# Optimization experiments

Hardware: AMD Instinct MI355X
Metric: run time of the kernel (lower is better)

## Reference

```python
import jax, jax.numpy as jnp
import numpy as np

B, S, H = 8, 8192, 1024
CAPACITY_FACTOR = 0.5


def setup_inputs() -> dict:
    key = jax.random.key(0)
    ks = jax.random.split(key, 5)
    sc = lambda fan: np.float32(1.0 / np.sqrt(fan))
    return {
        "x": jax.random.normal(ks[0], (B, S, H), dtype=jnp.float32),
        # router: Linear(H, H//4) -> ReLU -> Linear(H//4, 1)
        "W1": jax.random.normal(ks[1], (H, H // 4), dtype=jnp.float32) * sc(H),
        "b1": jnp.zeros((H // 4,), dtype=jnp.float32),
        "W2": jax.random.normal(ks[2], (H // 4, 1), dtype=jnp.float32) * sc(H // 4),
        "b2": jnp.zeros((1,), dtype=jnp.float32),
        # external layer_fn realized as a dense layer: gelu(x @ Wl)
        "Wl": jax.random.normal(ks[3], (H, H), dtype=jnp.float32) * sc(H),
    }


def reference(x, W1, b1, W2, b2, Wl):
    # router scores [B, S, 1]
    scores = jax.nn.relu(jnp.einsum("bsh,hd->bsd", x, W1) + b1)
    scores = jnp.einsum("bsd,do->bso", scores, W2) + b2
    routing_weights = jax.nn.sigmoid(scores)  # [B, S, 1]

    # eval path: process only top-capacity tokens per batch row
    capacity = int(S * CAPACITY_FACTOR)
    _, top_idx = jax.lax.top_k(scores[..., 0], capacity)  # [B, C]

    selected = jnp.take_along_axis(x, top_idx[..., None], axis=1)  # [B, C, H]
    processed = jax.nn.gelu(jnp.einsum("bch,hd->bcd", selected, Wl))  # layer_fn

    batch_idx = jnp.arange(x.shape[0])[:, None]  # [B, 1]
    output = x.at[batch_idx, top_idx].set(processed)  # scatter back into clone of x
    return output, routing_weights
```

## Files before the change

kernel.cpp:

```cpp
#include <hip/hip_runtime.h>
#include <stdint.h>

#define B_   8
#define S_   8192
#define H_   1024
#define HQ_  256
#define CAP_ 4096
#define UCAP_ (S_-CAP_)
#define M_   (B_*CAP_)
#define EPSB 0.012f
#define LCAP 8192

using f32x4 = __attribute__((ext_vector_type(4))) float;
using s16x8 = __attribute__((ext_vector_type(8))) short;

__device__ __forceinline__ unsigned short f2bf(float f) {
  unsigned u = __float_as_uint(f);
  u += 0x7FFF + ((u >> 16) & 1);
  return (unsigned short)(u >> 16);
}
__device__ __forceinline__ float bf2f(unsigned short h) {
  return __uint_as_float(((unsigned)h) << 16);
}

__device__ __forceinline__ float gelu_f(float v) {
  float s = v + 0.044715f * v * v * v;
  float e = __expf(-1.5957691216057308f * s);
  return v * __builtin_amdgcn_rcpf(1.0f + e);
}

__device__ __forceinline__ unsigned mono(float f) {
  unsigned u = __float_as_uint(f);
  return (u & 0x80000000u) ? ~u : (u | 0x80000000u);
}
__device__ __forceinline__ float unmono(unsigned k) {
  unsigned u = (k & 0x80000000u) ? (k & 0x7fffffffu) : ~k;
  return __uint_as_float(u);
}

__device__ __forceinline__ void gload_lds16(const void* g, void* l) {
  __builtin_amdgcn_global_load_lds(
      (const __attribute__((address_space(1))) void*)(uintptr_t)g,
      (__attribute__((address_space(3))) void*)(uintptr_t)l,
      16, 0, 0);
}

__device__ __forceinline__ float radix_select_T(
    const float* __restrict__ srow, unsigned* hist,
    unsigned* sh_b, unsigned* sh_gt, int tid) {
  unsigned prefix = 0; int plen = 0; unsigned rank = CAP_;
  #pragma unroll
  for (int round = 0; round < 3; ++round) {
    const int nb = (round < 2) ? 11 : 10;
    hist[tid] = 0; hist[tid + 1024] = 0;
    __syncthreads();
    for (int i = tid; i < S_; i += 1024) {
      unsigned k = mono(srow[i]);
      if (plen == 0 || (k >> (32 - plen)) == prefix) {
        unsigned bucket = (k << plen) >> (32 - nb);
        atomicAdd(&hist[bucket], 1u);
      }
    }
    __syncthreads();
    for (int s = 1; s < 2048; s <<= 1) {
      unsigned t0 = (tid + s < 2048) ? hist[tid + s] : 0;
      unsigned t1 = (tid + 1024 + s < 2048) ? hist[tid + 1024 + s] : 0;
      __syncthreads();
      hist[tid] += t0; hist[tid + 1024] += t1;
      __syncthreads();
    }
    #pragma unroll
    for (int h = 0; h < 2; ++h) {
      int i = tid + h * 1024;
      unsigned ge = hist[i];
      unsigned gt = (i < 2047) ? hist[i + 1] : 0;
      if (gt < rank && rank <= ge) { *sh_b = (unsigned)i; *sh_gt = gt; }
    }
    __syncthreads();
    prefix = (prefix << nb) | *sh_b;
    plen += nb;
    rank -= *sh_gt;
    __syncthreads();
  }
  return unmono(prefix);
}

__global__ __launch_bounds__(256) void prep_w1_kernel(
    const float* __restrict__ W1, unsigned short* __restrict__ w1t_hi) {
  __shared__ float tile[32][33];
  const int n0 = blockIdx.x * 32, k0 = blockIdx.y * 32;
  const int tx = threadIdx.x, ty = threadIdx.y;
  for (int i = ty; i < 32; i += 8) tile[i][tx] = W1[(size_t)(k0 + i) * HQ_ + n0 + tx];
  __syncthreads();
  for (int i = ty; i < 32; i += 8)
    w1t_hi[(size_t)(n0 + i) * H_ + k0 + tx] = f2bf(tile[tx][i]);
}

__global__ __launch_bounds__(512) void router_mfma_kernel(
    const float* __restrict__ x, const unsigned short* __restrict__ w1t_hi,
    const float* __restrict__ b1, const float* __restrict__ W2,
    const float* __restrict__ b2, float* __restrict__ scores,
    float* __restrict__ rw) {
  __shared__ __align__(16) unsigned short AsH[128 * 64];
  __shared__ __align__(16) unsigned short BsH[256 * 64];
  __shared__ float part[128][4];
  const int t = threadIdx.x;
  const int lane = t & 63, w = t >> 6;
  const int m0 = blockIdx.x * 128;
  const int wr = w >> 2, wc = w & 3;
  const int r16 = lane & 15, ks = lane >> 4;

  const float* aptr[4];
  int aso[4];
  #pragma unroll
  for (int u = 0; u < 4; ++u) {
    int idx = t + u * 512;
    int row = idx >> 4, q = idx & 15;
    aptr[u] = x + (size_t)(m0 + row) * H_ + q * 4;
    aso[u] = row * 64 + (((q >> 1) ^ (row & 7)) << 3) + (q & 1) * 4;
  }
  const unsigned short* bptr[4];
  int bdst[4];
  #pragma unroll
  for (int u = 0; u < 4; ++u) {
    int c0 = u * 512 + w * 64;
    int c = c0 + lane;
    int row = c >> 3, sl = c & 7;
    int slz = sl ^ (row & 7);
    bptr[u] = w1t_hi + (size_t)row * H_ + slz * 8;
    bdst[u] = c0 * 8;
  }

  f32x4 acc[4][4];
  #pragma unroll
  for (int i = 0; i < 4; ++i)
    #pragma unroll
    for (int j = 0; j < 4; ++j) acc[i][j] = (f32x4){0.f, 0.f, 0.f, 0.f};

  for (int k0 = 0; k0 < H_; k0 += 64) {
    float4 av[4];
    #pragma unroll
    for (int u = 0; u < 4; ++u) av[u] = *(const float4*)(aptr[u] + k0);
    #pragma unroll
    for (int u = 0; u < 4; ++u) gload_lds16(bptr[u] + k0, &BsH[bdst[u]]);
    #pragma unroll
    for (int u = 0; u < 4; ++u) {
      ushort4 hh;
      hh.x = f2bf(av[u].x); hh.y = f2bf(av[u].y);
      hh.z = f2bf(av[u].z); hh.w = f2bf(av[u].w);
      *(ushort4*)&AsH[aso[u]] = hh;
    }
    __syncthreads();
    #pragma unroll
    for (int kk = 0; kk < 2; ++kk) {
      const int g = kk * 4 + ks;
      s16x8 ah[4], bh[4];
      #pragma unroll
      for (int i = 0; i < 4; ++i) {
        int r = wr * 64 + i * 16 + r16;
        ah[i] = *(const s16x8*)&AsH[r * 64 + (g ^ (r & 7)) * 8];
      }
      #pragma unroll
      for (int j = 0; j < 4; ++j) {
        int r = wc * 64 + j * 16 + r16;
        bh[j] = *(const s16x8*)&BsH[r * 64 + (g ^ (r & 7)) * 8];
      }
      #pragma unroll
      for (int i = 0; i < 4; ++i)
        #pragma unroll
        for (int j = 0; j < 4; ++j)
          acc[i][j] = __builtin_amdgcn_mfma_f32_16x16x32_bf16(ah[i], bh[j], acc[i][j], 0, 0, 0);
    }
    __syncthreads();
  }

  float b1v[4], w2v[4];
  #pragma unroll
  for (int j = 0; j < 4; ++j) {
    int n = wc * 64 + j * 16 + r16;
    b1v[j] = b1[n]; w2v[j] = W2[n];
  }
  const int g4 = lane >> 4;
  #pragma unroll
  for (int i = 0; i < 4; ++i) {
    #pragma unroll
    for (int r = 0; r < 4; ++r) {
      float p = 0.f;
      #pragma unroll
      for (int j = 0; j < 4; ++j) {
        float h = acc[i][j][r] + b1v[j];
        h = fmaxf(h, 0.f);
        p = fmaf(h, w2v[j], p);
      }
      p += __shfl_xor(p, 1);
      p += __shfl_xor(p, 2);
      p += __shfl_xor(p, 4);
      p += __shfl_xor(p, 8);
      if (r16 == 0) part[wr * 64 + i * 16 + g4 * 4 + r][wc] = p;
    }
  }
  __syncthreads();
  if (t < 128) {
    float sc = part[t][0] + part[t][1] + part[t][2] + part[t][3] + b2[0];
    scores[m0 + t] = sc;
    rw[m0 + t] = 1.f / (1.f + expf(-sc));
  }
}

__global__ __launch_bounds__(1024) void select_band_kernel(
    const float* __restrict__ scores, int* __restrict__ list,
    int* __restrict__ count) {
  __shared__ unsigned hist[2048];
  __shared__ unsigned sh_b, sh_gt;
  const int b = blockIdx.x;
  const int tid = threadIdx.x;
  const float* srow = scores + (size_t)b * S_;
  const float T = radix_select_T(srow, hist, &sh_b, &sh_gt, tid);
  for (int i = tid; i < S_; i += 1024) {
    float s = srow[i];
    if (fabsf(s - T) <= EPSB) {
      int p = atomicAdd(count, 1);
      if (p < LCAP) list[p] = b * S_ + i;
    }
  }
}

__global__ __launch_bounds__(256) void recompute_kernel(
    const float* __restrict__ x, const float* __restrict__ W1,
    const float* __restrict__ b1, const float* __restrict__ W2,
    const float* __restrict__ b2, const int* __restrict__ list,
    const int* __restrict__ count, float* __restrict__ scores,
    float* __restrict__ rw) {
  __shared__ float xr[4][H_];
  __shared__ float red[4][4];
  int n = *count; if (n > LCAP) n = LCAP;
  const int j = threadIdx.x;
  for (int base = blockIdx.x * 4; base < n; base += gridDim.x * 4) {
    int nt = n - base; if (nt > 4) nt = 4;
    for (int tt = 0; tt < 4; ++tt) {
      int tok = list[base + ((tt < nt) ? tt : 0)];
      const float* xrow = x + (size_t)tok * H_;
      for (int k = j; k < H_; k += 256) xr[tt][k] = xrow[k];
    }
    __syncthreads();
    float a0 = 0.f, a1 = 0.f, a2 = 0.f, a3 = 0.f;
    for (int k = 0; k < H_; ++k) {
      float wv = W1[(size_t)k * HQ_ + j];
      a0 = fmaf(xr[0][k], wv, a0);
      a1 = fmaf(xr[1][k], wv, a1);
      a2 = fmaf(xr[2][k], wv, a2);
      a3 = fmaf(xr[3][k], wv, a3);
    }
    float aa[4] = {a0, a1, a2, a3};
    #pragma unroll
    for (int tt = 0; tt < 4; ++tt) {
      float h = fmaxf(aa[tt] + b1[j], 0.f);
      float v = h * W2[j];
      v += __shfl_xor(v, 1);  v += __shfl_xor(v, 2);  v += __shfl_xor(v, 4);
      v += __shfl_xor(v, 8);  v += __shfl_xor(v, 16); v += __shfl_xor(v, 32);
      if ((j & 63) == 0) red[tt][j >> 6] = v;
    }
    __syncthreads();
    if (j < nt) {
      int tok = list[base + j];
      float sc = red[j][0] + red[j][1] + red[j][2] + red[j][3] + b2[0];
      scores[tok] = sc;
      rw[tok] = 1.f / (1.f + expf(-sc));
    }
    __syncthreads();
  }
}

__global__ __launch_bounds__(1024) void compact_kernel(
    const float* __restrict__ scores, int* __restrict__ comp,
    int* __restrict__ ucomp) {
  __shared__ unsigned hist[2048];
  __shared__ unsigned sh_b, sh_gt;
  __shared__ int wc_eq[16], wc_sel[16], red[16];
  const int b = blockIdx.x;
  const float* srow = scores + (size_t)b * S_;
  const int tid = threadIdx.x, lane = tid & 63, wid = tid >> 6;
  const float T = radix_select_T(srow, hist, &sh_b, &sh_gt, tid);

  int cgt = 0;
  #pragma unroll
  for (int c = 0; c < 8; ++c) cgt += (srow[c * 1024 + tid] > T) ? 1 : 0;
  cgt += __shfl_xor(cgt, 1);  cgt += __shfl_xor(cgt, 2);  cgt += __shfl_xor(cgt, 4);
  cgt += __shfl_xor(cgt, 8);  cgt += __shfl_xor(cgt, 16); cgt += __shfl_xor(cgt, 32);
  if (lane == 0) red[wid] = cgt;
  __syncthreads();
  int cnt_gt = 0;
  #pragma unroll
  for (int i = 0; i < 16; ++i) cnt_gt += red[i];
  const int need = CAP_ - cnt_gt;

  int* crow = comp + b * CAP_;
  int* urow = ucomp + b * UCAP_;
  int sel_base = 0, unsel_base = 0, eq_base = 0;
  __syncthreads();
  for (int c = 0; c < 8; ++c) {
    int idx = c * 1024 + tid;
    float s = srow[idx];
    bool gt = s > T, eq = (s == T);
    unsigned long long meq = __ballot(eq);
    if (lane == 0) wc_eq[wid] = __popcll(meq);
    __syncthreads();
    int eq_off = eq_base, eq_tot = 0;
    #pragma unroll
    for (int w2 = 0; w2 < 16; ++w2) { if (w2 < wid) eq_off += wc_eq[w2]; eq_tot += wc_eq[w2]; }
    int eqpos = eq_off + __popcll(meq & ((1ull << lane) - 1));
    bool take = gt || (eq && eqpos < need);
    unsigned long long mt = __ballot(take);
    if (lane == 0) wc_sel[wid] = __popcll(mt);
    __syncthreads();
    int sel_off = sel_base, sel_tot = 0;
    #pragma unroll
    for (int w2 = 0; w2 < 16; ++w2) { if (w2 < wid) sel_off += wc_sel[w2]; sel_tot += wc_sel[w2]; }
    if (take) {
      crow[sel_off + __popcll(mt & ((1ull << lane) - 1))] = idx;
    } else {
      int un_off = unsel_base + wid * 64 - (sel_off - sel_base);
      urow[un_off + __popcll(~mt & ((1ull << lane) - 1))] = idx;
    }
    sel_base += sel_tot; unsel_base += 1024 - sel_tot; eq_base += eq_tot;
    __syncthreads();
  }
}

__global__ __launch_bounds__(256) void copy_unsel_kernel(
    const float* __restrict__ x, const int* __restrict__ ucomp,
    float* __restrict__ out) {
  int i = blockIdx.x;
  int b = i >> 12, r = i & (UCAP_ - 1);
  int token = ucomp[b * UCAP_ + r];
  size_t row = (size_t)b * S_ + token;
  const float4* src = (const float4*)(x + row * H_);
  float4* dst = (float4*)(out + row * H_);
  dst[threadIdx.x] = src[threadIdx.x];
}

__global__ __launch_bounds__(256) void wlt_kernel(
    const float* __restrict__ wl, unsigned short* __restrict__ wlt) {
  __shared__ float tile[32][33];
  const int x0 = blockIdx.x * 32, y0 = blockIdx.y * 32;
  const int tx = threadIdx.x, ty = threadIdx.y;
  for (int i = ty; i < 32; i += 8) tile[i][tx] = wl[(size_t)(y0 + i) * H_ + x0 + tx];
  __syncthreads();
  for (int i = ty; i < 32; i += 8)
    wlt[(size_t)(x0 + i) * H_ + y0 + tx] = f2bf(tile[tx][i]);
}

__global__ __launch_bounds__(256) void gather_cast_kernel(
    const float* __restrict__ x, const int* __restrict__ comp,
    unsigned short* __restrict__ xg) {
  int tid = blockIdx.x * 256 + threadIdx.x;
  int rowc = tid >> 8;
  int c4 = tid & 255;
  int b = rowc >> 12, cc = rowc & (CAP_ - 1);
  int token = comp[b * CAP_ + cc];
  float4 v = *(const float4*)&x[((size_t)(b * S_ + token)) * H_ + c4 * 4];
  ushort4 o;
  o.x = f2bf(v.x); o.y = f2bf(v.y); o.z = f2bf(v.z); o.w = f2bf(v.w);
  *(ushort4*)&xg[(size_t)rowc * H_ + c4 * 4] = o;
}

#define ISSUE_A(P, KT, BUF) do {                                               \
    int row_ = half * 128 + (P) * 32 + rr;                                     \
    int slz_ = sl ^ (row_ & 7);                                                \
    gload_lds16(xg + (size_t)(m0 + row_) * H_ + (KT) * 64 + slz_ * 8,          \
                &As[BUF][row_ * 64 + sl * 8]);                                 \
  } while (0)
#define ISSUE_B(P, KT, BUF) do {                                               \
    int row_ = half * 128 + (P) * 32 + rr;                                     \
    int slz_ = sl ^ (row_ & 7);                                                \
    gload_lds16(wlt + (size_t)(n0 + row_) * H_ + (KT) * 64 + slz_ * 8,         \
                &Bs[BUF][row_ * 64 + sl * 8]);                                 \
  } while (0)
#define MOE_PHASE(P, ISSUE, WAITSTR) do {                                      \
    s16x8 af[2][2];                                                            \
    _Pragma("unroll")                                                          \
    for (int i = 0; i < 2; ++i)                                                \
      _Pragma("unroll")                                                        \
      for (int kk = 0; kk < 2; ++kk) {                                         \
        int r_ = wr * 128 + (2 * (P) + i) * 16 + r16;                          \
        af[i][kk] = *(const s16x8*)&As[c_][r_ * 64 + ((kk * 4 + ks) ^ (r_ & 7)) * 8]; \
      }                                                                        \
    if ((P) == 0) {                                                            \
      _Pragma("unroll")                                                        \
      for (int j = 0; j < 4; ++j)                                              \
        _Pragma("unroll")                                                      \
        for (int kk = 0; kk < 2; ++kk) {                                       \
          int r_ = wc * 64 + j * 16 + r16;                                     \
          bfr[j][kk] = *(const s16x8*)&Bs[c_][r_ * 64 + ((kk * 4 + ks) ^ (r_ & 7)) * 8]; \
        }                                                                      \
    }                                                                          \
    ISSUE                                                                      \
    __builtin_amdgcn_s_barrier();                                              \
    asm volatile("s_waitcnt lgkmcnt(0)" ::: "memory");                         \
    __builtin_amdgcn_sched_barrier(0);                                         \
    __builtin_amdgcn_s_setprio(1);                                             \
    _Pragma("unroll")                                                          \
    for (int i = 0; i < 2; ++i)                                                \
      _Pragma("unroll")                                                        \
      for (int j = 0; j < 4; ++j)                                              \
        _Pragma("unroll")                                                      \
        for (int kk = 0; kk < 2; ++kk)                                         \
          acc[2 * (P) + i][j] = __builtin_amdgcn_mfma_f32_16x16x32_bf16(       \
              af[i][kk], bfr[j][kk], acc[2 * (P) + i][j], 0, 0, 0);            \
    __builtin_amdgcn_s_setprio(0);                                             \
    __builtin_amdgcn_sched_barrier(0);                                         \
    asm volatile("s_waitcnt " WAITSTR ::: "memory");                           \
    __builtin_amdgcn_s_barrier();                                              \
    __builtin_amdgcn_sched_barrier(0);                                         \
  } while (0)

__global__ __launch_bounds__(512, 1) void moe_gemm_kernel(
    const unsigned short* __restrict__ xg, const unsigned short* __restrict__ wlt,
    const int* __restrict__ comp, float* __restrict__ out) {
  __shared__ __align__(16) unsigned short As[2][256 * 64];
  __shared__ __align__(16) unsigned short Bs[2][256 * 64];
  __shared__ int toks[256];
  const int t = threadIdx.x;
  const int lane = t & 63, w = t >> 6;
  const int bid = blockIdx.x;
  const int xcd = bid & 7, wb = bid >> 3;
  const int m0 = (xcd * 16 + (wb >> 2)) * 256;
  const int n0 = (wb & 3) * 256;
  const int bb = m0 >> 12;
  if (t < 256) toks[t] = comp[bb * CAP_ + (m0 & (CAP_ - 1)) + t];
  const int wr = w >> 2, wc = w & 3;
  const int r16 = lane & 15, ks = lane >> 4;
  const int half = t >> 8, rr = (t >> 3) & 31, sl = t & 7;

  f32x4 acc[8][4];
  #pragma unroll
  for (int i = 0; i < 8; ++i)
    #pragma unroll
    for (int j = 0; j < 4; ++j) acc[i][j] = (f32x4){0.f, 0.f, 0.f, 0.f};

  ISSUE_B(0, 0, 0); ISSUE_B(1, 0, 0); ISSUE_B(2, 0, 0); ISSUE_B(3, 0, 0);
  ISSUE_A(0, 0, 0); ISSUE_A(1, 0, 0); ISSUE_A(2, 0, 0); ISSUE_A(3, 0, 0);
  asm volatile("s_waitcnt vmcnt(3)" ::: "memory");
  __syncthreads();

  for (int kt = 0; kt < 15; ++kt) {
    const int c_ = kt & 1, nb_ = c_ ^ 1;
    const int kn = kt + 1;
    s16x8 bfr[4][2];
    MOE_PHASE(0, { ISSUE_B(0, kn, nb_); ISSUE_B(1, kn, nb_); }, "vmcnt(4)");
    MOE_PHASE(1, { ISSUE_B(2, kn, nb_); ISSUE_B(3, kn, nb_); }, "vmcnt(5)");
    MOE_PHASE(2, { ISSUE_A(0, kn, nb_); ISSUE_A(1, kn, nb_); }, "vmcnt(6)");
    MOE_PHASE(3, { ISSUE_A(2, kn, nb_); ISSUE_A(3, kn, nb_); }, "vmcnt(3)");
  }
  {
    const int c_ = 1;
    s16x8 bfr[4][2];
    MOE_PHASE(0, {;}, "vmcnt(2)");
    MOE_PHASE(1, {;}, "vmcnt(1)");
    MOE_PHASE(2, {;}, "vmcnt(0)");
    MOE_PHASE(3, {;}, "vmcnt(63)");
  }

  const int g4 = lane >> 4;
  #pragma unroll
  for (int i = 0; i < 8; ++i) {
    #pragma unroll
    for (int r = 0; r < 4; ++r) {
      int rl = wr * 128 + i * 16 + g4 * 4 + r;
      int token = toks[rl];
      float* orow = out + ((size_t)(bb * S_ + token)) * H_ + n0 + wc * 64;
      #pragma unroll
      for (int j = 0; j < 4; ++j)
        orow[j * 16 + r16] = gelu_f(acc[i][j][r]);
    }
  }
}

extern "C" void kernel_launch(void* const* d_in, const int* in_sizes, int n_in,
                              void* d_out, int out_size, void* d_ws, size_t ws_size,
                              hipStream_t stream) {
  const float* x  = (const float*)d_in[0];
  const float* W1 = (const float*)d_in[1];
  const float* b1 = (const float*)d_in[2];
  const float* W2 = (const float*)d_in[3];
  const float* b2 = (const float*)d_in[4];
  const float* Wl = (const float*)d_in[5];
  float* out = (float*)d_out;
  float* rw  = out + (size_t)B_ * S_ * H_;

  char* ws = (char*)d_ws;
  float* scores        = (float*)ws;
  int*   comp          = (int*)(ws + (256 << 10));
  int*   count         = (int*)(ws + (384 << 10) + 256);
  int*   list          = (int*)(ws + (384 << 10) + 512);
  int*   ucomp         = (int*)(ws + (448 << 10));
  unsigned short* wlt  = (unsigned short*)(ws + (1 << 20));
  unsigned short* xg   = (unsigned short*)(ws + (3 << 20));
  unsigned short* w1t_hi = xg;

  hipMemsetAsync(count, 0, sizeof(int), stream);
  hipLaunchKernelGGL(prep_w1_kernel, dim3(HQ_/32, H_/32), dim3(32, 8), 0, stream,
                     W1, w1t_hi);
  hipLaunchKernelGGL(router_mfma_kernel, dim3((B_*S_)/128), dim3(512), 0, stream,
                     x, w1t_hi, b1, W2, b2, scores, rw);
  hipLaunchKernelGGL(select_band_kernel, dim3(B_), dim3(1024), 0, stream,
                     scores, list, count);
  hipLaunchKernelGGL(recompute_kernel, dim3(128), dim3(256), 0, stream,
                     x, W1, b1, W2, b2, list, count, scores, rw);
  hipLaunchKernelGGL(compact_kernel, dim3(B_), dim3(1024), 0, stream,
                     scores, comp, ucomp);
  hipLaunchKernelGGL(copy_unsel_kernel, dim3(B_*UCAP_), dim3(256), 0, stream,
                     x, ucomp, out);
  hipLaunchKernelGGL(wlt_kernel, dim3(H_/32, H_/32), dim3(32, 8), 0, stream, Wl, wlt);
  hipLaunchKernelGGL(gather_cast_kernel, dim3(M_*H_/4/256), dim3(256), 0, stream,
                     x, comp, xg);
  hipLaunchKernelGGL(moe_gemm_kernel, dim3((M_/256)*(H_/256)), dim3(512), 0, stream,
                     xg, wlt, comp, out);
}
```

Measured before the change: 395.6 us.

## Pipeline router GEMM with double-buffered direct-to-LDS loads and merge small kernels

The router GEMM now double-buffers both A (fp32 x, loaded directly to LDS and cast to bf16 at fragment-read time) and B tiles, using explicit vmcnt waits, barriers and setprio to overlap global loads with MFMA. The W1 and Wl transpose kernels are merged into one prep kernel, the gather/cast and unselected-row copy kernels are merged into one launch, and the count memset moves into the router kernel. This aims to hide memory latency in the router and cut launch overhead, at the cost of more LDS (fp32 A tile, two buffers) and occupancy limited to one block per CU.

```diff
diff --git a/kernel.cpp b/kernel.cpp
--- a/kernel.cpp
+++ b/kernel.cpp
@@ -85,93 +85,126 @@
   return unmono(prefix);
 }
 
-__global__ __launch_bounds__(256) void prep_w1_kernel(
-    const float* __restrict__ W1, unsigned short* __restrict__ w1t_hi) {
+__global__ __launch_bounds__(256) void prep_kernel(
+    const float* __restrict__ W1, unsigned short* __restrict__ w1t_hi,
+    const float* __restrict__ wl, unsigned short* __restrict__ wlt) {
   __shared__ float tile[32][33];
-  const int n0 = blockIdx.x * 32, k0 = blockIdx.y * 32;
+  const int bid = blockIdx.x;
   const int tx = threadIdx.x, ty = threadIdx.y;
-  for (int i = ty; i < 32; i += 8) tile[i][tx] = W1[(size_t)(k0 + i) * HQ_ + n0 + tx];
-  __syncthreads();
-  for (int i = ty; i < 32; i += 8)
-    w1t_hi[(size_t)(n0 + i) * H_ + k0 + tx] = f2bf(tile[tx][i]);
-}
-
-__global__ __launch_bounds__(512) void router_mfma_kernel(
+  if (bid < 256) {
+    int n0 = (bid & 7) * 32, k0 = (bid >> 3) * 32;
+    for (int i = ty; i < 32; i += 8) tile[i][tx] = W1[(size_t)(k0 + i) * HQ_ + n0 + tx];
+    __syncthreads();
+    for (int i = ty; i < 32; i += 8)
+      w1t_hi[(size_t)(n0 + i) * H_ + k0 + tx] = f2bf(tile[tx][i]);
+  } else {
+    int idx = bid - 256;
+    int x0 = (idx & 31) * 32, y0 = (idx >> 5) * 32;
+    for (int i = ty; i < 32; i += 8) tile[i][tx] = wl[(size_t)(y0 + i) * H_ + x0 + tx];
+    __syncthreads();
+    for (int i = ty; i < 32; i += 8)
+      wlt[(size_t)(x0 + i) * H_ + y0 + tx] = f2bf(tile[tx][i]);
+  }
+}
+
+#define RIA(U, KT, BUF) do {                                                   \
+    int c_i = (U) * 512 + t;                                                   \
+    int row_ = c_i >> 4, q_ = c_i & 15;                                        \
+    int qz_ = q_ ^ (row_ & 15);                                                \
+    gload_lds16(x + (size_t)(m0 + row_) * H_ + (KT) * 64 + qz_ * 4,            \
+                &Af[BUF][(size_t)c_i * 4]);                                    \
+  } while (0)
+#define RIB(U, KT, BUF) do {                                                   \
+    int row_ = (U) * 64 + (t >> 3);                                            \
+    int sl_ = t & 7;                                                           \
+    int slz_ = sl_ ^ (row_ & 7);                                               \
+    gload_lds16(w1t_hi + (size_t)row_ * H_ + (KT) * 64 + slz_ * 8,             \
+                &Bs[BUF][(size_t)row_ * 64 + sl_ * 8]);                        \
+  } while (0)
+#define RPH(P, ISSUE, WAITCODE) do {                                           \
+    s16x8 af[2];                                                               \
+    _Pragma("unroll")                                                          \
+    for (int kk = 0; kk < 2; ++kk) {                                           \
+      int r_ = wr * 64 + (P) * 16 + r16;                                       \
+      int g2 = 2 * (kk * 4 + ks);                                              \
+      float4 f0 = *(const float4*)&Af[c_][((size_t)r_ * 16 + (g2 ^ (r_ & 15))) * 4];       \
+      float4 f1 = *(const float4*)&Af[c_][((size_t)r_ * 16 + ((g2 + 1) ^ (r_ & 15))) * 4]; \
+      unsigned short hh[8];                                                    \
+      hh[0] = f2bf(f0.x); hh[1] = f2bf(f0.y); hh[2] = f2bf(f0.z); hh[3] = f2bf(f0.w); \
+      hh[4] = f2bf(f1.x); hh[5] = f2bf(f1.y); hh[6] = f2bf(f1.z); hh[7] = f2bf(f1.w); \
+      af[kk] = *(s16x8*)hh;                                                    \
+    }                                                                          \
+    if ((P) == 0) {                                                            \
+      _Pragma("unroll")                                                        \
+      for (int j = 0; j < 4; ++j)                                              \
+        _Pragma("unroll")                                                      \
+        for (int kk = 0; kk < 2; ++kk) {                                       \
+          int r_ = wc * 64 + j * 16 + r16;                                     \
+          bfr[j][kk] = *(const s16x8*)&Bs[c_][(size_t)r_ * 64 + ((kk * 4 + ks) ^ (r_ & 7)) * 8]; \
+        }                                                                      \
+    }                                                                          \
+    ISSUE                                                                      \
+    __builtin_amdgcn_s_barrier();                                              \
+    asm volatile("s_waitcnt lgkmcnt(0)" ::: "memory");                         \
+    __builtin_amdgcn_sched_barrier(0);                                         \
+    __builtin_amdgcn_s_setprio(1);                                             \
+    _Pragma("unroll")                                                          \
+    for (int j = 0; j < 4; ++j)                                                \
+      _Pragma("unroll")                                                        \
+      for (int kk = 0; kk < 2; ++kk)                                           \
+        acc[P][j] = __builtin_amdgcn_mfma_f32_16x16x32_bf16(                   \
+            af[kk], bfr[j][kk], acc[P][j], 0, 0, 0);                           \
+    __builtin_amdgcn_s_setprio(0);                                             \
+    __builtin_amdgcn_sched_barrier(0);                                         \
+    WAITCODE                                                                   \
+    __builtin_amdgcn_s_barrier();                                              \
+    __builtin_amdgcn_sched_barrier(0);                                         \
+  } while (0)
+
+__global__ __launch_bounds__(512, 1) void router_mfma_kernel(
     const float* __restrict__ x, const unsigned short* __restrict__ w1t_hi,
     const float* __restrict__ b1, const float* __restrict__ W2,
     const float* __restrict__ b2, float* __restrict__ scores,
-    float* __restrict__ rw) {
-  __shared__ __align__(16) unsigned short AsH[128 * 64];
-  __shared__ __align__(16) unsigned short BsH[256 * 64];
+    float* __restrict__ rw, int* __restrict__ count) {
+  __shared__ __align__(16) float Af[2][128 * 64];
+  __shared__ __align__(16) unsigned short Bs[2][256 * 64];
   __shared__ float part[128][4];
   const int t = threadIdx.x;
   const int lane = t & 63, w = t >> 6;
   const int m0 = blockIdx.x * 128;
+  if (blockIdx.x == 0 && t == 0) *count = 0;
   const int wr = w >> 2, wc = w & 3;
   const int r16 = lane & 15, ks = lane >> 4;
 
-  const float* aptr[4];
-  int aso[4];
-  #pragma unroll
-  for (int u = 0; u < 4; ++u) {
-    int idx = t + u * 512;
-    int row = idx >> 4, q = idx & 15;
-    aptr[u] = x + (size_t)(m0 + row) * H_ + q * 4;
-    aso[u] = row * 64 + (((q >> 1) ^ (row & 7)) << 3) + (q & 1) * 4;
-  }
-  const unsigned short* bptr[4];
-  int bdst[4];
-  #pragma unroll
-  for (int u = 0; u < 4; ++u) {
-    int c0 = u * 512 + w * 64;
-    int c = c0 + lane;
-    int row = c >> 3, sl = c & 7;
-    int slz = sl ^ (row & 7);
-    bptr[u] = w1t_hi + (size_t)row * H_ + slz * 8;
-    bdst[u] = c0 * 8;
-  }
-
   f32x4 acc[4][4];
   #pragma unroll
   for (int i = 0; i < 4; ++i)
     #pragma unroll
     for (int j = 0; j < 4; ++j) acc[i][j] = (f32x4){0.f, 0.f, 0.f, 0.f};
 
-  for (int k0 = 0; k0 < H_; k0 += 64) {
-    float4 av[4];
-    #pragma unroll
-    for (int u = 0; u < 4; ++u) av[u] = *(const float4*)(aptr[u] + k0);
-    #pragma unroll
-    for (int u = 0; u < 4; ++u) gload_lds16(bptr[u] + k0, &BsH[bdst[u]]);
-    #pragma unroll
-    for (int u = 0; u < 4; ++u) {
-      ushort4 hh;
-      hh.x = f2bf(av[u].x); hh.y = f2bf(av[u].y);
-      hh.z = f2bf(av[u].z); hh.w = f2bf(av[u].w);
-      *(ushort4*)&AsH[aso[u]] = hh;
-    }
-    __syncthreads();
-    #pragma unroll
-    for (int kk = 0; kk < 2; ++kk) {
-      const int g = kk * 4 + ks;
-      s16x8 ah[4], bh[4];
-      #pragma unroll
-      for (int i = 0; i < 4; ++i) {
-        int r = wr * 64 + i * 16 + r16;
-        ah[i] = *(const s16x8*)&AsH[r * 64 + (g ^ (r & 7)) * 8];
-      }
-      #pragma unroll
-      for (int j = 0; j < 4; ++j) {
-        int r = wc * 64 + j * 16 + r16;
-        bh[j] = *(const s16x8*)&BsH[r * 64 + (g ^ (r & 7)) * 8];
-      }
-      #pragma unroll
-      for (int i = 0; i < 4; ++i)
-        #pragma unroll
-        for (int j = 0; j < 4; ++j)
-          acc[i][j] = __builtin_amdgcn_mfma_f32_16x16x32_bf16(ah[i], bh[j], acc[i][j], 0, 0, 0);
-    }
-    __syncthreads();
+  RIB(0, 0, 0); RIB(1, 0, 0); RIB(2, 0, 0); RIB(3, 0, 0);
+  RIA(0, 0, 0); RIA(2, 0, 0); RIA(1, 0, 0); RIA(3, 0, 0);
+  asm volatile("s_waitcnt vmcnt(2)" ::: "memory");
+  __syncthreads();
+
+  for (int kt = 0; kt < 15; ++kt) {
+    const int c_ = kt & 1, nb_ = c_ ^ 1;
+    const int kn = kt + 1;
+    s16x8 bfr[4][2];
+    RPH(0, { RIB(0, kn, nb_); RIB(1, kn, nb_); }, {});
+    RPH(1, { RIB(2, kn, nb_); RIB(3, kn, nb_); },
+        { asm volatile("s_waitcnt vmcnt(4)" ::: "memory"); });
+    RPH(2, { RIA(0, kn, nb_); RIA(2, kn, nb_); }, {});
+    RPH(3, { RIA(1, kn, nb_); RIA(3, kn, nb_); },
+        { asm volatile("s_waitcnt vmcnt(2)" ::: "memory"); });
+  }
+  {
+    const int c_ = 1;
+    s16x8 bfr[4][2];
+    RPH(0, {;}, {});
+    RPH(1, {;}, { asm volatile("s_waitcnt vmcnt(0)" ::: "memory"); });
+    RPH(2, {;}, {});
+    RPH(3, {;}, {});
   }
 
   float b1v[4], w2v[4];
@@ -327,41 +360,26 @@
   }
 }
 
-__global__ __launch_bounds__(256) void copy_unsel_kernel(
-    const float* __restrict__ x, const int* __restrict__ ucomp,
+__global__ __launch_bounds__(256) void gather_copy_kernel(
+    const float* __restrict__ x, const int* __restrict__ comp,
+    const int* __restrict__ ucomp, unsigned short* __restrict__ xg,
     float* __restrict__ out) {
-  int i = blockIdx.x;
-  int b = i >> 12, r = i & (UCAP_ - 1);
-  int token = ucomp[b * UCAP_ + r];
-  size_t row = (size_t)b * S_ + token;
-  const float4* src = (const float4*)(x + row * H_);
-  float4* dst = (float4*)(out + row * H_);
-  dst[threadIdx.x] = src[threadIdx.x];
-}
-
-__global__ __launch_bounds__(256) void wlt_kernel(
-    const float* __restrict__ wl, unsigned short* __restrict__ wlt) {
-  __shared__ float tile[32][33];
-  const int x0 = blockIdx.x * 32, y0 = blockIdx.y * 32;
-  const int tx = threadIdx.x, ty = threadIdx.y;
-  for (int i = ty; i < 32; i += 8) tile[i][tx] = wl[(size_t)(y0 + i) * H_ + x0 + tx];
-  __syncthreads();
-  for (int i = ty; i < 32; i += 8)
-    wlt[(size_t)(x0 + i) * H_ + y0 + tx] = f2bf(tile[tx][i]);
-}
-
-__global__ __launch_bounds__(256) void gather_cast_kernel(
-    const float* __restrict__ x, const int* __restrict__ comp,
-    unsigned short* __restrict__ xg) {
-  int tid = blockIdx.x * 256 + threadIdx.x;
-  int rowc = tid >> 8;
-  int c4 = tid & 255;
-  int b = rowc >> 12, cc = rowc & (CAP_ - 1);
-  int token = comp[b * CAP_ + cc];
-  float4 v = *(const float4*)&x[((size_t)(b * S_ + token)) * H_ + c4 * 4];
-  ushort4 o;
-  o.x = f2bf(v.x); o.y = f2bf(v.y); o.z = f2bf(v.z); o.w = f2bf(v.w);
-  *(ushort4*)&xg[(size_t)rowc * H_ + c4 * 4] = o;
+  const int bid = blockIdx.x;
+  const int tx = threadIdx.x;
+  if (bid < M_) {
+    int b = bid >> 12, cc = bid & (CAP_ - 1);
+    int token = comp[b * CAP_ + cc];
+    float4 v = ((const float4*)(x + ((size_t)(b * S_ + token)) * H_))[tx];
+    ushort4 o;
+    o.x = f2bf(v.x); o.y = f2bf(v.y); o.z = f2bf(v.z); o.w = f2bf(v.w);
+    *(ushort4*)&xg[(size_t)bid * H_ + tx * 4] = o;
+  } else {
+    int i = bid - M_;
+    int b = i >> 12, r = i & (UCAP_ - 1);
+    int token = ucomp[b * UCAP_ + r];
+    size_t row = (size_t)b * S_ + token;
+    ((float4*)(out + row * H_))[tx] = ((const float4*)(x + row * H_))[tx];
+  }
 }
 
 #define ISSUE_A(P, KT, BUF) do {                                               \
@@ -498,22 +516,18 @@
   unsigned short* xg   = (unsigned short*)(ws + (3 << 20));
   unsigned short* w1t_hi = xg;
 
-  hipMemsetAsync(count, 0, sizeof(int), stream);
-  hipLaunchKernelGGL(prep_w1_kernel, dim3(HQ_/32, H_/32), dim3(32, 8), 0, stream,
-                     W1, w1t_hi);
+  hipLaunchKernelGGL(prep_kernel, dim3(1280), dim3(32, 8), 0, stream,
+                     W1, w1t_hi, Wl, wlt);
   hipLaunchKernelGGL(router_mfma_kernel, dim3((B_*S_)/128), dim3(512), 0, stream,
-                     x, w1t_hi, b1, W2, b2, scores, rw);
+                     x, w1t_hi, b1, W2, b2, scores, rw, count);
   hipLaunchKernelGGL(select_band_kernel, dim3(B_), dim3(1024), 0, stream,
                      scores, list, count);
   hipLaunchKernelGGL(recompute_kernel, dim3(128), dim3(256), 0, stream,
                      x, W1, b1, W2, b2, list, count, scores, rw);
   hipLaunchKernelGGL(compact_kernel, dim3(B_), dim3(1024), 0, stream,
                      scores, comp, ucomp);
-  hipLaunchKernelGGL(copy_unsel_kernel, dim3(B_*UCAP_), dim3(256), 0, stream,
-                     x, ucomp, out);
-  hipLaunchKernelGGL(wlt_kernel, dim3(H_/32, H_/32), dim3(32, 8), 0, stream, Wl, wlt);
-  hipLaunchKernelGGL(gather_cast_kernel, dim3(M_*H_/4/256), dim3(256), 0, stream,
-                     x, comp, xg);
+  hipLaunchKernelGGL(gather_copy_kernel, dim3(M_ + B_*UCAP_), dim3(256), 0, stream,
+                     x, comp, ucomp, xg, out);
   hipLaunchKernelGGL(moe_gemm_kernel, dim3((M_/256)*(H_/256)), dim3(512), 0, stream,
                      xg, wlt, comp, out);
 }
```

Result: no change. 390.2 us (-1.3%).

## Merge prep, gather and copy kernels; restage router tiles with async fp32 loads

Applied to the files above, without the earlier changes.

The W1 and Wl transpose-cast kernels become one launch, and the gather-cast and unselected-row copy become one launch. The memset of the count is folded into the router kernel. The router kernel now uses 256 threads over 64-row tiles, loading fp32 x straight into LDS with async global-to-LDS copies using a swizzled layout, and converts to bf16 when reading fragments. This removes three launches and the register round-trip for A, in exchange for more LDS per block and repeated bf16 conversion in each wave.

```diff
diff --git a/kernel.cpp b/kernel.cpp
--- a/kernel.cpp
+++ b/kernel.cpp
@@ -85,50 +85,61 @@
   return unmono(prefix);
 }
 
-__global__ __launch_bounds__(256) void prep_w1_kernel(
-    const float* __restrict__ W1, unsigned short* __restrict__ w1t_hi) {
+__global__ __launch_bounds__(256) void prep_kernel(
+    const float* __restrict__ W1, unsigned short* __restrict__ w1t_hi,
+    const float* __restrict__ wl, unsigned short* __restrict__ wlt) {
   __shared__ float tile[32][33];
-  const int n0 = blockIdx.x * 32, k0 = blockIdx.y * 32;
+  const int bid = blockIdx.x;
   const int tx = threadIdx.x, ty = threadIdx.y;
-  for (int i = ty; i < 32; i += 8) tile[i][tx] = W1[(size_t)(k0 + i) * HQ_ + n0 + tx];
-  __syncthreads();
-  for (int i = ty; i < 32; i += 8)
-    w1t_hi[(size_t)(n0 + i) * H_ + k0 + tx] = f2bf(tile[tx][i]);
-}
-
-__global__ __launch_bounds__(512) void router_mfma_kernel(
+  if (bid < 256) {
+    int n0 = (bid & 7) * 32, k0 = (bid >> 3) * 32;
+    for (int i = ty; i < 32; i += 8) tile[i][tx] = W1[(size_t)(k0 + i) * HQ_ + n0 + tx];
+    __syncthreads();
+    for (int i = ty; i < 32; i += 8)
+      w1t_hi[(size_t)(n0 + i) * H_ + k0 + tx] = f2bf(tile[tx][i]);
+  } else {
+    int idx = bid - 256;
+    int x0 = (idx & 31) * 32, y0 = (idx >> 5) * 32;
+    for (int i = ty; i < 32; i += 8) tile[i][tx] = wl[(size_t)(y0 + i) * H_ + x0 + tx];
+    __syncthreads();
+    for (int i = ty; i < 32; i += 8)
+      wlt[(size_t)(x0 + i) * H_ + y0 + tx] = f2bf(tile[tx][i]);
+  }
+}
+
+__global__ __launch_bounds__(256) void router_mfma_kernel(
     const float* __restrict__ x, const unsigned short* __restrict__ w1t_hi,
     const float* __restrict__ b1, const float* __restrict__ W2,
     const float* __restrict__ b2, float* __restrict__ scores,
-    float* __restrict__ rw) {
-  __shared__ __align__(16) unsigned short AsH[128 * 64];
-  __shared__ __align__(16) unsigned short BsH[256 * 64];
-  __shared__ float part[128][4];
+    float* __restrict__ rw, int* __restrict__ count) {
+  __shared__ __align__(16) float Af[64 * 64];
+  __shared__ __align__(16) unsigned short Bs[256 * 64];
+  __shared__ float part[64][4];
   const int t = threadIdx.x;
   const int lane = t & 63, w = t >> 6;
-  const int m0 = blockIdx.x * 128;
-  const int wr = w >> 2, wc = w & 3;
+  const int m0 = blockIdx.x * 64;
+  if (blockIdx.x == 0 && t == 0) *count = 0;
   const int r16 = lane & 15, ks = lane >> 4;
 
-  const float* aptr[4];
-  int aso[4];
+  const float* aP[4];
+  int adst[4];
   #pragma unroll
   for (int u = 0; u < 4; ++u) {
-    int idx = t + u * 512;
-    int row = idx >> 4, q = idx & 15;
-    aptr[u] = x + (size_t)(m0 + row) * H_ + q * 4;
-    aso[u] = row * 64 + (((q >> 1) ^ (row & 7)) << 3) + (q & 1) * 4;
-  }
-  const unsigned short* bptr[4];
-  int bdst[4];
-  #pragma unroll
-  for (int u = 0; u < 4; ++u) {
-    int c0 = u * 512 + w * 64;
-    int c = c0 + lane;
+    int c = u * 256 + t;
+    int row = c >> 4, q = c & 15;
+    int qz = q ^ (row & 15);
+    aP[u] = x + (size_t)(m0 + row) * H_ + qz * 4;
+    adst[u] = c * 4;
+  }
+  const unsigned short* bP[8];
+  int bdst[8];
+  #pragma unroll
+  for (int u = 0; u < 8; ++u) {
+    int c = u * 256 + t;
     int row = c >> 3, sl = c & 7;
     int slz = sl ^ (row & 7);
-    bptr[u] = w1t_hi + (size_t)row * H_ + slz * 8;
-    bdst[u] = c0 * 8;
+    bP[u] = w1t_hi + (size_t)row * H_ + slz * 8;
+    bdst[u] = c * 8;
   }
 
   f32x4 acc[4][4];
@@ -138,46 +149,47 @@
     for (int j = 0; j < 4; ++j) acc[i][j] = (f32x4){0.f, 0.f, 0.f, 0.f};
 
   for (int k0 = 0; k0 < H_; k0 += 64) {
-    float4 av[4];
-    #pragma unroll
-    for (int u = 0; u < 4; ++u) av[u] = *(const float4*)(aptr[u] + k0);
-    #pragma unroll
-    for (int u = 0; u < 4; ++u) gload_lds16(bptr[u] + k0, &BsH[bdst[u]]);
-    #pragma unroll
-    for (int u = 0; u < 4; ++u) {
-      ushort4 hh;
-      hh.x = f2bf(av[u].x); hh.y = f2bf(av[u].y);
-      hh.z = f2bf(av[u].z); hh.w = f2bf(av[u].w);
-      *(ushort4*)&AsH[aso[u]] = hh;
-    }
-    __syncthreads();
-    #pragma unroll
-    for (int kk = 0; kk < 2; ++kk) {
-      const int g = kk * 4 + ks;
-      s16x8 ah[4], bh[4];
+    #pragma unroll
+    for (int u = 0; u < 4; ++u) gload_lds16(aP[u] + k0, &Af[adst[u]]);
+    #pragma unroll
+    for (int u = 0; u < 8; ++u) gload_lds16(bP[u] + k0, &Bs[bdst[u]]);
+    __syncthreads();
+    s16x8 af[4][2], bfr[4][2];
+    #pragma unroll
+    for (int i = 0; i < 4; ++i)
       #pragma unroll
-      for (int i = 0; i < 4; ++i) {
-        int r = wr * 64 + i * 16 + r16;
-        ah[i] = *(const s16x8*)&AsH[r * 64 + (g ^ (r & 7)) * 8];
+      for (int kk = 0; kk < 2; ++kk) {
+        int r_ = i * 16 + r16;
+        int g2 = 2 * (kk * 4 + ks);
+        float4 f0 = *(const float4*)&Af[(r_ * 16 + (g2 ^ (r_ & 15))) * 4];
+        float4 f1 = *(const float4*)&Af[(r_ * 16 + ((g2 + 1) ^ (r_ & 15))) * 4];
+        unsigned short hh[8];
+        hh[0] = f2bf(f0.x); hh[1] = f2bf(f0.y); hh[2] = f2bf(f0.z); hh[3] = f2bf(f0.w);
+        hh[4] = f2bf(f1.x); hh[5] = f2bf(f1.y); hh[6] = f2bf(f1.z); hh[7] = f2bf(f1.w);
+        af[i][kk] = *(s16x8*)hh;
       }
+    #pragma unroll
+    for (int j = 0; j < 4; ++j)
       #pragma unroll
-      for (int j = 0; j < 4; ++j) {
-        int r = wc * 64 + j * 16 + r16;
-        bh[j] = *(const s16x8*)&BsH[r * 64 + (g ^ (r & 7)) * 8];
+      for (int kk = 0; kk < 2; ++kk) {
+        int r_ = w * 64 + j * 16 + r16;
+        bfr[j][kk] = *(const s16x8*)&Bs[r_ * 64 + ((kk * 4 + ks) ^ (r_ & 7)) * 8];
       }
+    #pragma unroll
+    for (int i = 0; i < 4; ++i)
       #pragma unroll
-      for (int i = 0; i < 4; ++i)
+      for (int j = 0; j < 4; ++j)
         #pragma unroll
-        for (int j = 0; j < 4; ++j)
-          acc[i][j] = __builtin_amdgcn_mfma_f32_16x16x32_bf16(ah[i], bh[j], acc[i][j], 0, 0, 0);
-    }
+        for (int kk = 0; kk < 2; ++kk)
+          acc[i][j] = __builtin_amdgcn_mfma_f32_16x16x32_bf16(
+              af[i][kk], bfr[j][kk], acc[i][j], 0, 0, 0);
     __syncthreads();
   }
 
   float b1v[4], w2v[4];
   #pragma unroll
   for (int j = 0; j < 4; ++j) {
-    int n = wc * 64 + j * 16 + r16;
+    int n = w * 64 + j * 16 + r16;
     b1v[j] = b1[n]; w2v[j] = W2[n];
   }
   const int g4 = lane >> 4;
@@ -196,11 +208,11 @@
       p += __shfl_xor(p, 2);
       p += __shfl_xor(p, 4);
       p += __shfl_xor(p, 8);
-      if (r16 == 0) part[wr * 64 + i * 16 + g4 * 4 + r][wc] = p;
+      if (r16 == 0) part[i * 16 + g4 * 4 + r][w] = p;
     }
   }
   __syncthreads();
-  if (t < 128) {
+  if (t < 64) {
     float sc = part[t][0] + part[t][1] + part[t][2] + part[t][3] + b2[0];
     scores[m0 + t] = sc;
     rw[m0 + t] = 1.f / (1.f + expf(-sc));
@@ -327,41 +339,26 @@
   }
 }
 
-__global__ __launch_bounds__(256) void copy_unsel_kernel(
-    const float* __restrict__ x, const int* __restrict__ ucomp,
+__global__ __launch_bounds__(256) void gather_copy_kernel(
+    const float* __restrict__ x, const int* __restrict__ comp,
+    const int* __restrict__ ucomp, unsigned short* __restrict__ xg,
     float* __restrict__ out) {
-  int i = blockIdx.x;
-  int b = i >> 12, r = i & (UCAP_ - 1);
-  int token = ucomp[b * UCAP_ + r];
-  size_t row = (size_t)b * S_ + token;
-  const float4* src = (const float4*)(x + row * H_);
-  float4* dst = (float4*)(out + row * H_);
-  dst[threadIdx.x] = src[threadIdx.x];
-}
-
-__global__ __launch_bounds__(256) void wlt_kernel(
-    const float* __restrict__ wl, unsigned short* __restrict__ wlt) {
-  __shared__ float tile[32][33];
-  const int x0 = blockIdx.x * 32, y0 = blockIdx.y * 32;
-  const int tx = threadIdx.x, ty = threadIdx.y;
-  for (int i = ty; i < 32; i += 8) tile[i][tx] = wl[(size_t)(y0 + i) * H_ + x0 + tx];
-  __syncthreads();
-  for (int i = ty; i < 32; i += 8)
-    wlt[(size_t)(x0 + i) * H_ + y0 + tx] = f2bf(tile[tx][i]);
-}
-
-__global__ __launch_bounds__(256) void gather_cast_kernel(
-    const float* __restrict__ x, const int* __restrict__ comp,
-    unsigned short* __restrict__ xg) {
-  int tid = blockIdx.x * 256 + threadIdx.x;
-  int rowc = tid >> 8;
-  int c4 = tid & 255;
-  int b = rowc >> 12, cc = rowc & (CAP_ - 1);
-  int token = comp[b * CAP_ + cc];
-  float4 v = *(const float4*)&x[((size_t)(b * S_ + token)) * H_ + c4 * 4];
-  ushort4 o;
-  o.x = f2bf(v.x); o.y = f2bf(v.y); o.z = f2bf(v.z); o.w = f2bf(v.w);
-  *(ushort4*)&xg[(size_t)rowc * H_ + c4 * 4] = o;
+  const int bid = blockIdx.x;
+  const int tx = threadIdx.x;
+  if (bid < M_) {
+    int b = bid >> 12, cc = bid & (CAP_ - 1);
+    int token = comp[b * CAP_ + cc];
+    float4 v = ((const float4*)(x + ((size_t)(b * S_ + token)) * H_))[tx];
+    ushort4 o;
+    o.x = f2bf(v.x); o.y = f2bf(v.y); o.z = f2bf(v.z); o.w = f2bf(v.w);
+    *(ushort4*)&xg[(size_t)bid * H_ + tx * 4] = o;
+  } else {
+    int i = bid - M_;
+    int b = i >> 12, r = i & (UCAP_ - 1);
+    int token = ucomp[b * UCAP_ + r];
+    size_t row = (size_t)b * S_ + token;
+    ((float4*)(out + row * H_))[tx] = ((const float4*)(x + row * H_))[tx];
+  }
 }
 
 #define ISSUE_A(P, KT, BUF) do {                                               \
@@ -498,22 +495,18 @@
   unsigned short* xg   = (unsigned short*)(ws + (3 << 20));
   unsigned short* w1t_hi = xg;
 
-  hipMemsetAsync(count, 0, sizeof(int), stream);
-  hipLaunchKernelGGL(prep_w1_kernel, dim3(HQ_/32, H_/32), dim3(32, 8), 0, stream,
-                     W1, w1t_hi);
-  hipLaunchKernelGGL(router_mfma_kernel, dim3((B_*S_)/128), dim3(512), 0, stream,
-                     x, w1t_hi, b1, W2, b2, scores, rw);
+  hipLaunchKernelGGL(prep_kernel, dim3(1280), dim3(32, 8), 0, stream,
+                     W1, w1t_hi, Wl, wlt);
+  hipLaunchKernelGGL(router_mfma_kernel, dim3((B_*S_)/64), dim3(256), 0, stream,
+                     x, w1t_hi, b1, W2, b2, scores, rw, count);
   hipLaunchKernelGGL(select_band_kernel, dim3(B_), dim3(1024), 0, stream,
                      scores, list, count);
   hipLaunchKernelGGL(recompute_kernel, dim3(128), dim3(256), 0, stream,
                      x, W1, b1, W2, b2, list, count, scores, rw);
   hipLaunchKernelGGL(compact_kernel, dim3(B_), dim3(1024), 0, stream,
                      scores, comp, ucomp);
-  hipLaunchKernelGGL(copy_unsel_kernel, dim3(B_*UCAP_), dim3(256), 0, stream,
-                     x, ucomp, out);
-  hipLaunchKernelGGL(wlt_kernel, dim3(H_/32, H_/32), dim3(32, 8), 0, stream, Wl, wlt);
-  hipLaunchKernelGGL(gather_cast_kernel, dim3(M_*H_/4/256), dim3(256), 0, stream,
-                     x, comp, xg);
+  hipLaunchKernelGGL(gather_copy_kernel, dim3(M_ + B_*UCAP_), dim3(256), 0, stream,
+                     x, comp, ucomp, xg, out);
   hipLaunchKernelGGL(moe_gemm_kernel, dim3((M_/256)*(H_/256)), dim3(512), 0, stream,
                      xg, wlt, comp, out);
 }
```

New measurement: 422.9 us. +6.9%, slower.
